# Performance work log

Measured on AMD Instinct MI355X. Metric: run time of the kernel, lower is better.

## Reference

```python
import jax, jax.numpy as jnp
import numpy as np

N_HEADS = 16


def _apply_rope(x, cos, sin):
    # x: (B, T, H, hd); cos/sin: (max_len, hd//2)
    B, T, H, hd = x.shape
    c = cos[:T][None, :, None, :]  # (1, T, 1, hd//2)
    s = sin[:T][None, :, None, :]
    x1 = x[..., 0::2]
    x2 = x[..., 1::2]
    y1 = x1 * c - x2 * s
    y2 = x1 * s + x2 * c
    return jnp.stack((y1, y2), axis=-1).reshape(B, T, H, hd)


def _precompute_rope(head_dim, max_len):
    theta = 10000.0
    inv = 1.0 / theta ** (np.arange(0, head_dim, 2, dtype=np.float32) / head_dim)
    t = np.arange(max_len, dtype=np.float32)
    freqs = np.outer(t, inv)
    return jnp.asarray(np.cos(freqs)), jnp.asarray(np.sin(freqs))


def setup_inputs() -> dict:
    key = jax.random.key(0)
    k1, k2, k3 = jax.random.split(key, 3)
    B, T, C = 4, 2048, 2048
    hd = C // N_HEADS
    x = jax.random.normal(k1, (B, T, C), dtype=jnp.float32)
    w_attn = jax.random.normal(k2, (C, 3 * C), dtype=jnp.float32) * (C ** -0.5)
    w_proj = jax.random.normal(k3, (C, C), dtype=jnp.float32) * (C ** -0.5)
    rope_cos, rope_sin = _precompute_rope(hd, T)
    return {"x": x, "w_attn": w_attn, "w_proj": w_proj,
            "rope_cos": rope_cos, "rope_sin": rope_sin}


def reference(x, w_attn, w_proj, rope_cos, rope_sin):
    B, T, C = x.shape
    H = N_HEADS
    hd = C // H
    qkv = x @ w_attn  # (B, T, 3C)
    q, k, v = jnp.split(qkv, 3, axis=2)
    q = q.reshape(B, T, H, hd)
    k = k.reshape(B, T, H, hd)
    v = v.reshape(B, T, H, hd)
    q = _apply_rope(q, rope_cos, rope_sin)
    k = _apply_rope(k, rope_cos, rope_sin)
    scale = 1.0 / jnp.sqrt(jnp.asarray(hd, dtype=x.dtype))
    scores = jnp.einsum('bqhd,bkhd->bhqk', q, k) * scale  # (B, H, T, T)
    causal = jnp.tril(jnp.ones((T, T), dtype=bool))
    scores = jnp.where(causal[None, None], scores, jnp.finfo(scores.dtype).min)
    attn = jax.nn.softmax(scores, axis=-1)
    y = jnp.einsum('bhqk,bkhd->bqhd', attn, v).reshape(B, T, C)
    return y @ w_proj
```

## Files before the change

kernel.cpp:

```cpp
#include <hip/hip_runtime.h>
#include <cstdint>
#include <cstddef>

#define DEVI __device__ __forceinline__

typedef __attribute__((ext_vector_type(8))) short bf16x8;
typedef __attribute__((ext_vector_type(4))) float f32x4;

DEVI unsigned short f2bf(float f) {
  unsigned int u = __float_as_uint(f);
  u += 0x7fffu + ((u >> 16) & 1u);
  return (unsigned short)(u >> 16);
}
DEVI float bf2f(unsigned int us) { return __uint_as_float(us << 16); }

DEVI void gld_lds16(const void* g, void* l) {
  __builtin_amdgcn_global_load_lds(
      (const __attribute__((address_space(1))) void*)g,
      (__attribute__((address_space(3))) void*)l, 16, 0, 0);
}

__global__ __launch_bounds__(256) void k_conv(const float* __restrict__ in,
                                              short* __restrict__ out, int n4) {
  int i = blockIdx.x * 256 + threadIdx.x;
  if (i >= n4) return;
  float4 v = reinterpret_cast<const float4*>(in)[i];
  uint2 o;
  o.x = (unsigned)f2bf(v.x) | ((unsigned)f2bf(v.y) << 16);
  o.y = (unsigned)f2bf(v.z) | ((unsigned)f2bf(v.w) << 16);
  reinterpret_cast<uint2*>(out)[i] = o;
}

__global__ __launch_bounds__(256) void k_transpose(const float* __restrict__ in,
                                                   short* __restrict__ out,
                                                   int R, int Cc) {
  __shared__ short tile[64][66];
  int tcols = Cc >> 6;
  int tb = blockIdx.x % tcols;
  int rb = blockIdx.x / tcols;
  int tid = threadIdx.x;
#pragma unroll
  for (int rep = 0; rep < 16; ++rep) {
    int idx = rep * 256 + tid;
    int r = idx >> 6, c = idx & 63;
    tile[r][c] = (short)f2bf(in[(size_t)(rb * 64 + r) * Cc + tb * 64 + c]);
  }
  __syncthreads();
#pragma unroll
  for (int rep = 0; rep < 16; ++rep) {
    int idx = rep * 256 + tid;
    int r = idx >> 6, c = idx & 63;
    out[(size_t)(tb * 64 + r) * R + rb * 64 + c] = tile[c][r];
  }
}

template <typename OutT>
__global__ __launch_bounds__(512, 2) void k_gemm8(const short* __restrict__ A,
                                                  const short* __restrict__ BT,
                                                  OutT* __restrict__ C,
                                                  int M, int N, int K) {
  __shared__ short sA[4][8192];
  __shared__ short sB[4][8192];
  const int tid = threadIdx.x;
  const int wv = tid >> 6, lane = tid & 63;
  const int l16 = lane & 15, lhi = lane >> 4;
  const int wr = wv >> 2, wc = wv & 3;
  const int bm = blockIdx.x * 256, bn = blockIdx.y * 256;

  const int srow0 = wv * 16 + (lane >> 2);
  const int sgs = lane & 3;

  auto stageA = [&](int kt, int b) {
#pragma unroll
    for (int j = 0; j < 2; ++j) {
      int row = j * 128 + srow0;
      int g = sgs ^ ((row >> 1) & 3);
      gld_lds16(A + (size_t)(bm + row) * K + kt + g * 8,
                &sA[b][j * 4096 + wv * 512]);
    }
  };
  auto stageB = [&](int kt, int b) {
#pragma unroll
    for (int j = 0; j < 2; ++j) {
      int row = j * 128 + srow0;
      int g = sgs ^ ((row >> 1) & 3);
      gld_lds16(BT + (size_t)(bn + row) * K + kt + g * 8,
                &sB[b][j * 4096 + wv * 512]);
    }
  };

  f32x4 acc[8][4] = {};
  const int NT = K >> 5;

  stageA(0, 0); stageB(0, 0);
  stageA(32, 1); stageB(32, 1);
  asm volatile("s_waitcnt vmcnt(4)" ::: "memory");
  __builtin_amdgcn_s_barrier();
  asm volatile("" ::: "memory");

  for (int t = 0; t < NT; ++t) {
    const int cur = t & 3;
    const int nb = (t + 2) & 3;
    bf16x8 bfr[4], af[4];
#pragma unroll
    for (int n = 0; n < 4; ++n) {
      int row = wc * 64 + n * 16 + l16;
      bfr[n] = *(const bf16x8*)&sB[cur][row * 32 + (lhi ^ ((row >> 1) & 3)) * 8];
    }
#pragma unroll
    for (int m = 0; m < 4; ++m) {
      int row = wr * 128 + m * 16 + l16;
      af[m] = *(const bf16x8*)&sA[cur][row * 32 + (lhi ^ ((row >> 1) & 3)) * 8];
    }
    if (t + 2 < NT) stageA((t + 2) * 32, nb);
    __builtin_amdgcn_s_barrier();
    asm volatile("s_waitcnt lgkmcnt(0)" ::: "memory");
    __builtin_amdgcn_s_setprio(1);
#pragma unroll
    for (int m = 0; m < 4; ++m)
#pragma unroll
      for (int n = 0; n < 4; ++n)
        acc[m][n] = __builtin_amdgcn_mfma_f32_16x16x32_bf16(af[m], bfr[n],
                                                            acc[m][n], 0, 0, 0);
    __builtin_amdgcn_s_setprio(0);
    __builtin_amdgcn_s_barrier();
    asm volatile("" ::: "memory");
#pragma unroll
    for (int m = 0; m < 4; ++m) {
      int row = wr * 128 + 64 + m * 16 + l16;
      af[m] = *(const bf16x8*)&sA[cur][row * 32 + (lhi ^ ((row >> 1) & 3)) * 8];
    }
    if (t + 2 < NT) {
      stageB((t + 2) * 32, nb);
      asm volatile("s_waitcnt vmcnt(4)" ::: "memory");
    } else if (t + 1 < NT) {
      asm volatile("s_waitcnt vmcnt(0)" ::: "memory");
    }
    __builtin_amdgcn_s_barrier();
    asm volatile("s_waitcnt lgkmcnt(0)" ::: "memory");
    __builtin_amdgcn_s_setprio(1);
#pragma unroll
    for (int m = 0; m < 4; ++m)
#pragma unroll
      for (int n = 0; n < 4; ++n)
        acc[m + 4][n] = __builtin_amdgcn_mfma_f32_16x16x32_bf16(af[m], bfr[n],
                                                                acc[m + 4][n],
                                                                0, 0, 0);
    __builtin_amdgcn_s_setprio(0);
    __builtin_amdgcn_s_barrier();
    asm volatile("" ::: "memory");
  }

#pragma unroll
  for (int m = 0; m < 8; ++m) {
#pragma unroll
    for (int n = 0; n < 4; ++n) {
      int col = bn + wc * 64 + n * 16 + l16;
#pragma unroll
      for (int r = 0; r < 4; ++r) {
        int row = bm + wr * 128 + m * 16 + lhi * 4 + r;
        if constexpr (sizeof(OutT) == 2)
          C[(size_t)row * N + col] = (OutT)f2bf(acc[m][n][r]);
        else
          C[(size_t)row * N + col] = acc[m][n][r];
      }
    }
  }
}

__global__ __launch_bounds__(256) void k_rope(const short* __restrict__ qkv,
                                              const float* __restrict__ cosb,
                                              const float* __restrict__ sinb,
                                              short* __restrict__ Qr,
                                              short* __restrict__ Kr) {
  const float kC = 0.08838834764831845f * 1.44269504088896340f;
  int gid = blockIdx.x * 4 + (threadIdx.x >> 6);
  int lane = threadIdx.x & 63;
  int h = gid & 15;
  int bt = gid >> 4;
  int t = bt & 2047;
  int b = bt >> 11;
  float c = cosb[t * 64 + lane];
  float s = sinb[t * 64 + lane];
  size_t qidx = (size_t)bt * 6144 + h * 128 + 2 * lane;
  size_t oidx = ((size_t)(b * 16 + h) * 2048 + t) * 128 + 2 * lane;
  unsigned int qp = *reinterpret_cast<const unsigned int*>(qkv + qidx);
  {
    float x1 = bf2f(qp & 0xffffu), x2 = bf2f(qp >> 16);
    unsigned int o = (unsigned)f2bf((x1 * c - x2 * s) * kC) |
                     ((unsigned)f2bf((x1 * s + x2 * c) * kC) << 16);
    *reinterpret_cast<unsigned int*>(Qr + oidx) = o;
  }
  unsigned int kp = *reinterpret_cast<const unsigned int*>(qkv + qidx + 2048);
  {
    float x1 = bf2f(kp & 0xffffu), x2 = bf2f(kp >> 16);
    unsigned int o = (unsigned)f2bf(x1 * c - x2 * s) |
                     ((unsigned)f2bf(x1 * s + x2 * c) << 16);
    *reinterpret_cast<unsigned int*>(Kr + oidx) = o;
  }
}

__global__ __launch_bounds__(256) void k_vtrans(const short* __restrict__ qkv,
                                                short* __restrict__ VT) {
  __shared__ short tile[64][66];
  int bh = blockIdx.x;
  int t0 = blockIdx.y * 64;
  int d0 = blockIdx.z * 64;
  int b = bh >> 4, h = bh & 15;
  int tid = threadIdx.x;
#pragma unroll
  for (int rep = 0; rep < 16; ++rep) {
    int idx = rep * 256 + tid;
    int r = idx >> 6, c = idx & 63;
    tile[r][c] = qkv[(size_t)(b * 2048 + t0 + r) * 6144 + 4096 + h * 128 + d0 + c];
  }
  __syncthreads();
#pragma unroll
  for (int rep = 0; rep < 16; ++rep) {
    int idx = rep * 256 + tid;
    int r = idx >> 6, c = idx & 63;
    VT[(size_t)(bh * 128 + d0 + r) * 2048 + t0 + c] = tile[c][r];
  }
}

__global__ __launch_bounds__(256) void k_attn(const short* __restrict__ Qr,
                                              const short* __restrict__ Kr,
                                              const short* __restrict__ VT,
                                              short* __restrict__ Y) {
  __shared__ short sK[2][64 * 128];
  __shared__ short sVT[2][128 * 64];
  __shared__ short sP[4][16 * 64];
  const int tid = threadIdx.x, wv = tid >> 6, lane = tid & 63;
  const int l8r = lane >> 3, l8c = lane & 7, l16 = lane & 15, lhi = lane >> 4;
  const int bid = blockIdx.x;
  const int pair = bid & 15, bh = bid >> 4;
  const size_t base = (size_t)bh * 2048 * 128;
  const int b = bh >> 4, h = bh & 15;

  const short ob = (short)0x3F80;
  const bf16x8 ones = {ob, ob, ob, ob, ob, ob, ob, ob};

  auto stage = [&](int kv0, int buf) {
#pragma unroll
    for (int rr = 0; rr < 4; ++rr) {
      int ch = rr * 4 + wv;
      {
        int row = ch * 4 + lhi;
        int wch = l16 ^ (row & 7);
        gld_lds16(Kr + base + (size_t)(kv0 + row) * 128 + wch * 8,
                  &sK[buf][ch * 512]);
      }
      {
        int drow = ch * 8 + l8r;
        int wch = l8c ^ (drow & 7);
        gld_lds16(VT + base + (size_t)drow * 2048 + kv0 + wch * 8,
                  &sVT[buf][ch * 512]);
      }
    }
  };

  for (int half = 0; half < 2; ++half) {
    const int qt = half ? 31 - pair : pair;
    const int q0 = qt * 64;
    const int nt = qt + 1;

    bf16x8 qf[4];
    const int qrow = q0 + wv * 16 + l16;
#pragma unroll
    for (int ks = 0; ks < 4; ++ks)
      qf[ks] = *reinterpret_cast<const bf16x8*>(Qr + base + (size_t)qrow * 128 +
                                                ks * 32 + lhi * 8);

    f32x4 acc_o[8] = {};
    f32x4 acc_l = {};
    float m_run[4];
#pragma unroll
    for (int r = 0; r < 4; ++r) m_run[r] = -1e30f;

    stage(0, 0);
    __syncthreads();

    for (int it = 0; it < nt; ++it) {
      const int cur = it & 1;
      if (it + 1 < nt) stage((it + 1) * 64, cur ^ 1);

      f32x4 sacc[4] = {};
#pragma unroll
      for (int cf = 0; cf < 4; ++cf) {
        int krow = cf * 16 + l16;
#pragma unroll
        for (int ks = 0; ks < 4; ++ks) {
          int e = krow * 128 + ks * 32 + lhi * 8;
          bf16x8 kf = *reinterpret_cast<const bf16x8*>(
              &sK[cur][e ^ ((krow & 7) << 3)]);
          sacc[cf] = __builtin_amdgcn_mfma_f32_16x16x32_bf16(qf[ks], kf,
                                                             sacc[cf], 0, 0, 0);
        }
      }

      if (it == nt - 1) {
#pragma unroll
        for (int cf = 0; cf < 4; ++cf) {
          int col = cf * 16 + l16;
#pragma unroll
          for (int r = 0; r < 4; ++r)
            if (col > wv * 16 + lhi * 4 + r) sacc[cf][r] = -3e38f;
        }
      }

      bool exceed = false;
#pragma unroll
      for (int cf = 0; cf < 4; ++cf)
#pragma unroll
        for (int r = 0; r < 4; ++r)
          exceed |= (sacc[cf][r] > m_run[r] + 8.f);

      if (__any(exceed)) {
        float resc[4];
#pragma unroll
        for (int r = 0; r < 4; ++r) {
          float mx = fmaxf(fmaxf(sacc[0][r], sacc[1][r]),
                           fmaxf(sacc[2][r], sacc[3][r]));
          mx = fmaxf(mx, __shfl_xor(mx, 1));
          mx = fmaxf(mx, __shfl_xor(mx, 2));
          mx = fmaxf(mx, __shfl_xor(mx, 4));
          mx = fmaxf(mx, __shfl_xor(mx, 8));
          float mnew = fmaxf(m_run[r], mx);
          resc[r] = exp2f(m_run[r] - mnew);
          m_run[r] = mnew;
        }
#pragma unroll
        for (int df = 0; df < 8; ++df)
#pragma unroll
          for (int r = 0; r < 4; ++r) acc_o[df][r] *= resc[r];
#pragma unroll
        for (int r = 0; r < 4; ++r) acc_l[r] *= resc[r];
      }

#pragma unroll
      for (int cf = 0; cf < 4; ++cf)
#pragma unroll
        for (int r = 0; r < 4; ++r) {
          float p = exp2f(sacc[cf][r] - m_run[r]);
          int prow = lhi * 4 + r;
          int e = prow * 64 + cf * 16 + l16;
          sP[wv][e ^ ((prow & 7) << 3)] = (short)f2bf(p);
        }

#pragma unroll
      for (int kk = 0; kk < 2; ++kk) {
        int e = l16 * 64 + kk * 32 + lhi * 8;
        bf16x8 pa = *reinterpret_cast<const bf16x8*>(
            &sP[wv][e ^ ((l16 & 7) << 3)]);
        acc_l = __builtin_amdgcn_mfma_f32_16x16x32_bf16(pa, ones, acc_l, 0, 0, 0);
#pragma unroll
        for (int df = 0; df < 8; ++df) {
          int vrow = df * 16 + l16;
          int ev = vrow * 64 + kk * 32 + lhi * 8;
          bf16x8 vb = *reinterpret_cast<const bf16x8*>(
              &sVT[cur][ev ^ ((vrow & 7) << 3)]);
          acc_o[df] = __builtin_amdgcn_mfma_f32_16x16x32_bf16(pa, vb,
                                                              acc_o[df], 0, 0, 0);
        }
      }
      __syncthreads();
    }

    float inv[4];
#pragma unroll
    for (int r = 0; r < 4; ++r) inv[r] = 1.f / acc_l[r];
#pragma unroll
    for (int df = 0; df < 8; ++df) {
      int col = h * 128 + df * 16 + l16;
#pragma unroll
      for (int r = 0; r < 4; ++r) {
        int row = q0 + wv * 16 + lhi * 4 + r;
        Y[((size_t)b * 2048 + row) * 2048 + col] =
            (short)f2bf(acc_o[df][r] * inv[r]);
      }
    }
  }
}

extern "C" void kernel_launch(void* const* d_in, const int* in_sizes, int n_in,
                              void* d_out, int out_size, void* d_ws, size_t ws_size,
                              hipStream_t stream) {
  const float* x        = (const float*)d_in[0];
  const float* w_attn   = (const float*)d_in[1];
  const float* w_proj   = (const float*)d_in[2];
  const float* rope_cos = (const float*)d_in[3];
  const float* rope_sin = (const float*)d_in[4];

  char* ws = (char*)d_ws;
  short* xbf    = (short*)(ws);
  short* wattnT = (short*)(ws + 33554432ull);
  short* wprojT = (short*)(ws + 58720256ull);
  short* qkv    = (short*)(ws + 67108864ull);
  short* Y      = qkv;
  short* Qr     = (short*)(ws + 167772160ull);
  short* Kr     = (short*)(ws + 201326592ull);
  short* VT     = (short*)(ws + 234881024ull);

  k_conv<<<16384, 256, 0, stream>>>(x, xbf, 4194304);
  k_transpose<<<3072, 256, 0, stream>>>(w_attn, wattnT, 2048, 6144);
  k_transpose<<<1024, 256, 0, stream>>>(w_proj, wprojT, 2048, 2048);
  k_gemm8<short><<<dim3(32, 24), 512, 0, stream>>>(xbf, wattnT, qkv,
                                                   8192, 6144, 2048);
  k_rope<<<32768, 256, 0, stream>>>(qkv, rope_cos, rope_sin, Qr, Kr);
  k_vtrans<<<dim3(64, 32, 2), 256, 0, stream>>>(qkv, VT);
  k_attn<<<1024, 256, 0, stream>>>(Qr, Kr, VT, Y);
  k_gemm8<float><<<dim3(32, 8), 512, 0, stream>>>(Y, wprojT, (float*)d_out,
                                                  8192, 2048, 2048);
}
```

Baseline: 514.2 us.

## Double-buffer GEMM fragments in registers with deeper LDS prefetch

Reworks the bf16 GEMM main loop. The LDS stage now prefetches three k-tiles ahead instead of two, and each k-tile's full A and B fragments are loaded into a second register set while the MFMAs for the current tile run from the first set. The loop is unrolled by two so the two register sets alternate, cutting the four barriers and LDS-read stalls per k-tile down to one barrier. The cost is higher register pressure from two full fragment sets next to the 8x4 accumulators, which risks spills or lower occupancy. It also assumes the number of k-tiles is even.

```diff
diff --git a/kernel.cpp b/kernel.cpp
--- a/kernel.cpp
+++ b/kernel.cpp
@@ -66,9 +66,9 @@
   const int l16 = lane & 15, lhi = lane >> 4;
   const int wr = wv >> 2, wc = wv & 3;
   const int bm = blockIdx.x * 256, bn = blockIdx.y * 256;
-
   const int srow0 = wv * 16 + (lane >> 2);
   const int sgs = lane & 3;
+  const int NT = K >> 5;
 
   auto stageA = [&](int kt, int b) {
 #pragma unroll
@@ -90,66 +90,64 @@
   };
 
   f32x4 acc[8][4] = {};
-  const int NT = K >> 5;
+  bf16x8 aP[8], bP[4], aQ[8], bQ[4];
+
+#define FRAG_READ(DA, DB, BUF)                                                 \
+  {                                                                            \
+    const short* bufA_ = sA[(BUF)];                                            \
+    const short* bufB_ = sB[(BUF)];                                            \
+    _Pragma("unroll") for (int n = 0; n < 4; ++n) {                            \
+      int row = wc * 64 + n * 16 + l16;                                        \
+      DB[n] = *(const bf16x8*)&bufB_[row * 32 + ((lhi ^ ((row >> 1) & 3)) << 3)]; \
+    }                                                                          \
+    _Pragma("unroll") for (int m = 0; m < 8; ++m) {                            \
+      int row = wr * 128 + m * 16 + l16;                                       \
+      DA[m] = *(const bf16x8*)&bufA_[row * 32 + ((lhi ^ ((row >> 1) & 3)) << 3)]; \
+    }                                                                          \
+  }
+
+#define TILE_BODY(T, CA, CB, NA, NB)                                           \
+  {                                                                            \
+    const int t_ = (T);                                                        \
+    if (t_ + 1 < NT) FRAG_READ(NA, NB, (t_ + 1) & 3);                          \
+    if (t_ + 3 < NT) {                                                         \
+      stageA((t_ + 3) * 32, (t_ + 3) & 3);                                     \
+      stageB((t_ + 3) * 32, (t_ + 3) & 3);                                     \
+    }                                                                          \
+    __builtin_amdgcn_sched_barrier(0);                                         \
+    if (t_ + 3 < NT) {                                                         \
+      asm volatile("s_waitcnt vmcnt(4)" ::: "memory");                         \
+    } else {                                                                   \
+      asm volatile("s_waitcnt vmcnt(0)" ::: "memory");                         \
+    }                                                                          \
+    __builtin_amdgcn_sched_barrier(0);                                         \
+    __builtin_amdgcn_s_setprio(1);                                             \
+    _Pragma("unroll") for (int m = 0; m < 8; ++m)                              \
+        _Pragma("unroll") for (int n = 0; n < 4; ++n)                          \
+            acc[m][n] = __builtin_amdgcn_mfma_f32_16x16x32_bf16(               \
+                CA[m], CB[n], acc[m][n], 0, 0, 0);                             \
+    __builtin_amdgcn_s_setprio(0);                                             \
+    __builtin_amdgcn_sched_barrier(0);                                         \
+    __builtin_amdgcn_s_barrier();                                              \
+    __builtin_amdgcn_sched_barrier(0);                                         \
+  }
 
   stageA(0, 0); stageB(0, 0);
   stageA(32, 1); stageB(32, 1);
+  stageA(64, 2); stageB(64, 2);
+  asm volatile("s_waitcnt vmcnt(8)" ::: "memory");
+  __builtin_amdgcn_s_barrier();
+  FRAG_READ(aP, bP, 0);
   asm volatile("s_waitcnt vmcnt(4)" ::: "memory");
   __builtin_amdgcn_s_barrier();
-  asm volatile("" ::: "memory");
-
-  for (int t = 0; t < NT; ++t) {
-    const int cur = t & 3;
-    const int nb = (t + 2) & 3;
-    bf16x8 bfr[4], af[4];
-#pragma unroll
-    for (int n = 0; n < 4; ++n) {
-      int row = wc * 64 + n * 16 + l16;
-      bfr[n] = *(const bf16x8*)&sB[cur][row * 32 + (lhi ^ ((row >> 1) & 3)) * 8];
-    }
-#pragma unroll
-    for (int m = 0; m < 4; ++m) {
-      int row = wr * 128 + m * 16 + l16;
-      af[m] = *(const bf16x8*)&sA[cur][row * 32 + (lhi ^ ((row >> 1) & 3)) * 8];
-    }
-    if (t + 2 < NT) stageA((t + 2) * 32, nb);
-    __builtin_amdgcn_s_barrier();
-    asm volatile("s_waitcnt lgkmcnt(0)" ::: "memory");
-    __builtin_amdgcn_s_setprio(1);
-#pragma unroll
-    for (int m = 0; m < 4; ++m)
-#pragma unroll
-      for (int n = 0; n < 4; ++n)
-        acc[m][n] = __builtin_amdgcn_mfma_f32_16x16x32_bf16(af[m], bfr[n],
-                                                            acc[m][n], 0, 0, 0);
-    __builtin_amdgcn_s_setprio(0);
-    __builtin_amdgcn_s_barrier();
-    asm volatile("" ::: "memory");
-#pragma unroll
-    for (int m = 0; m < 4; ++m) {
-      int row = wr * 128 + 64 + m * 16 + l16;
-      af[m] = *(const bf16x8*)&sA[cur][row * 32 + (lhi ^ ((row >> 1) & 3)) * 8];
-    }
-    if (t + 2 < NT) {
-      stageB((t + 2) * 32, nb);
-      asm volatile("s_waitcnt vmcnt(4)" ::: "memory");
-    } else if (t + 1 < NT) {
-      asm volatile("s_waitcnt vmcnt(0)" ::: "memory");
-    }
-    __builtin_amdgcn_s_barrier();
-    asm volatile("s_waitcnt lgkmcnt(0)" ::: "memory");
-    __builtin_amdgcn_s_setprio(1);
-#pragma unroll
-    for (int m = 0; m < 4; ++m)
-#pragma unroll
-      for (int n = 0; n < 4; ++n)
-        acc[m + 4][n] = __builtin_amdgcn_mfma_f32_16x16x32_bf16(af[m], bfr[n],
-                                                                acc[m + 4][n],
-                                                                0, 0, 0);
-    __builtin_amdgcn_s_setprio(0);
-    __builtin_amdgcn_s_barrier();
-    asm volatile("" ::: "memory");
-  }
+  __builtin_amdgcn_sched_barrier(0);
+
+  for (int t = 0; t < NT; t += 2) {
+    TILE_BODY(t, aP, bP, aQ, bQ);
+    TILE_BODY(t + 1, aQ, bQ, aP, bP);
+  }
+#undef FRAG_READ
+#undef TILE_BODY
 
 #pragma unroll
   for (int m = 0; m < 8; ++m) {
```

New measurement: 496.0 us. -3.5%, faster.

## Restructure GEMM mainloop to process two K-tiles per barrier pair

Applied to the files above, without the earlier changes.

Rewrites the bf16 GEMM main loop so each iteration issues global-to-LDS loads for the next two K-tiles up front, then computes two full K-tiles (all 8x4 MFMAs each) before a single vmcnt(0) wait and barrier. It replaces the earlier ping-pong schedule, which had four barriers per tile and interleaved half-tile A fragment loads. The aim is fewer barriers and less sync overhead per K step. In exchange it holds 8 A fragments live (more registers) and waits on all outstanding loads at the end of each pair, which may expose memory latency.

```diff
diff --git a/kernel.cpp b/kernel.cpp
--- a/kernel.cpp
+++ b/kernel.cpp
@@ -66,9 +66,9 @@
   const int l16 = lane & 15, lhi = lane >> 4;
   const int wr = wv >> 2, wc = wv & 3;
   const int bm = blockIdx.x * 256, bn = blockIdx.y * 256;
-
   const int srow0 = wv * 16 + (lane >> 2);
   const int sgs = lane & 3;
+  const int NT = K >> 5;
 
   auto stageA = [&](int kt, int b) {
 #pragma unroll
@@ -90,65 +90,44 @@
   };
 
   f32x4 acc[8][4] = {};
-  const int NT = K >> 5;
 
   stageA(0, 0); stageB(0, 0);
   stageA(32, 1); stageB(32, 1);
-  asm volatile("s_waitcnt vmcnt(4)" ::: "memory");
+  asm volatile("s_waitcnt vmcnt(0)" ::: "memory");
   __builtin_amdgcn_s_barrier();
-  asm volatile("" ::: "memory");
-
-  for (int t = 0; t < NT; ++t) {
-    const int cur = t & 3;
-    const int nb = (t + 2) & 3;
-    bf16x8 bfr[4], af[4];
-#pragma unroll
-    for (int n = 0; n < 4; ++n) {
-      int row = wc * 64 + n * 16 + l16;
-      bfr[n] = *(const bf16x8*)&sB[cur][row * 32 + (lhi ^ ((row >> 1) & 3)) * 8];
-    }
-#pragma unroll
-    for (int m = 0; m < 4; ++m) {
-      int row = wr * 128 + m * 16 + l16;
-      af[m] = *(const bf16x8*)&sA[cur][row * 32 + (lhi ^ ((row >> 1) & 3)) * 8];
-    }
-    if (t + 2 < NT) stageA((t + 2) * 32, nb);
+
+  for (int t = 0; t < NT; t += 2) {
+    if (t + 2 < NT) { stageA((t + 2) * 32, (t + 2) & 3);
+                      stageB((t + 2) * 32, (t + 2) & 3); }
+    if (t + 3 < NT) { stageA((t + 3) * 32, (t + 3) & 3);
+                      stageB((t + 3) * 32, (t + 3) & 3); }
+    __builtin_amdgcn_sched_barrier(0);
+#pragma unroll
+    for (int u = 0; u < 2; ++u) {
+      const short* bufA = sA[(t + u) & 3];
+      const short* bufB = sB[(t + u) & 3];
+      bf16x8 bfr[4], af[8];
+#pragma unroll
+      for (int n = 0; n < 4; ++n) {
+        int row = wc * 64 + n * 16 + l16;
+        bfr[n] = *(const bf16x8*)&bufB[row * 32 + ((lhi ^ ((row >> 1) & 3)) << 3)];
+      }
+#pragma unroll
+      for (int m = 0; m < 8; ++m) {
+        int row = wr * 128 + m * 16 + l16;
+        af[m] = *(const bf16x8*)&bufA[row * 32 + ((lhi ^ ((row >> 1) & 3)) << 3)];
+      }
+      __builtin_amdgcn_s_setprio(1);
+#pragma unroll
+      for (int m = 0; m < 8; ++m)
+#pragma unroll
+        for (int n = 0; n < 4; ++n)
+          acc[m][n] = __builtin_amdgcn_mfma_f32_16x16x32_bf16(af[m], bfr[n],
+                                                              acc[m][n], 0, 0, 0);
+      __builtin_amdgcn_s_setprio(0);
+    }
+    asm volatile("s_waitcnt vmcnt(0)" ::: "memory");
     __builtin_amdgcn_s_barrier();
-    asm volatile("s_waitcnt lgkmcnt(0)" ::: "memory");
-    __builtin_amdgcn_s_setprio(1);
-#pragma unroll
-    for (int m = 0; m < 4; ++m)
-#pragma unroll
-      for (int n = 0; n < 4; ++n)
-        acc[m][n] = __builtin_amdgcn_mfma_f32_16x16x32_bf16(af[m], bfr[n],
-                                                            acc[m][n], 0, 0, 0);
-    __builtin_amdgcn_s_setprio(0);
-    __builtin_amdgcn_s_barrier();
-    asm volatile("" ::: "memory");
-#pragma unroll
-    for (int m = 0; m < 4; ++m) {
-      int row = wr * 128 + 64 + m * 16 + l16;
-      af[m] = *(const bf16x8*)&sA[cur][row * 32 + (lhi ^ ((row >> 1) & 3)) * 8];
-    }
-    if (t + 2 < NT) {
-      stageB((t + 2) * 32, nb);
-      asm volatile("s_waitcnt vmcnt(4)" ::: "memory");
-    } else if (t + 1 < NT) {
-      asm volatile("s_waitcnt vmcnt(0)" ::: "memory");
-    }
-    __builtin_amdgcn_s_barrier();
-    asm volatile("s_waitcnt lgkmcnt(0)" ::: "memory");
-    __builtin_amdgcn_s_setprio(1);
-#pragma unroll
-    for (int m = 0; m < 4; ++m)
-#pragma unroll
-      for (int n = 0; n < 4; ++n)
-        acc[m + 4][n] = __builtin_amdgcn_mfma_f32_16x16x32_bf16(af[m], bfr[n],
-                                                                acc[m + 4][n],
-                                                                0, 0, 0);
-    __builtin_amdgcn_s_setprio(0);
-    __builtin_amdgcn_s_barrier();
-    asm volatile("" ::: "memory");
   }
 
 #pragma unroll
```

Result: slower. 550.8 us (+7.1%).
